# Kernel tuning notes

Hardware: AMD Instinct MI355X
Metric: run time of the kernel (lower is better)

## Reference

```python
import jax, jax.numpy as jnp
import numpy as np

L, C, H = 12, 1024, 16  # n_layer, n_embd, n_head
D = C // H
EPS = 1e-5

def gelu_new(x):
    # GPT-2 tanh-approximate GELU
    return 0.5 * x * (1.0 + jnp.tanh(np.sqrt(2.0 / np.pi).astype(np.float32) * (x + 0.044715 * x ** 3)))

def layernorm(x, g, b):
    mu = jnp.mean(x, axis=-1, keepdims=True)
    var = jnp.mean(jnp.square(x - mu), axis=-1, keepdims=True)
    return (x - mu) * jax.lax.rsqrt(var + EPS) * g + b

def setup_inputs() -> dict:
    key = jax.random.key(0)
    ks = jax.random.split(key, 8)
    std = 0.02
    inp = {
        'inputs_embeds': jax.random.normal(ks[0], (1, 1024, C), jnp.float32),
        'attention_mask': jnp.ones((1, 1024), jnp.float32),
        'ln1_g': jnp.ones((L, C), jnp.float32), 'ln1_b': jnp.zeros((L, C), jnp.float32),
        'Wqkv': jax.random.normal(ks[1], (L, C, 3 * C), jnp.float32) * std,
        'bqkv': jnp.zeros((L, 3 * C), jnp.float32),
        'Wo': jax.random.normal(ks[2], (L, C, C), jnp.float32) * (std / np.sqrt(2 * L)),
        'bo': jnp.zeros((L, C), jnp.float32),
        'ln2_g': jnp.ones((L, C), jnp.float32), 'ln2_b': jnp.zeros((L, C), jnp.float32),
        'Wfc': jax.random.normal(ks[3], (L, C, 4 * C), jnp.float32) * std,
        'bfc': jnp.zeros((L, 4 * C), jnp.float32),
        'Wmp': jax.random.normal(ks[4], (L, 4 * C, C), jnp.float32) * (std / np.sqrt(2 * L)),
        'bmp': jnp.zeros((L, C), jnp.float32),
        'lnf_g': jnp.ones((C,), jnp.float32), 'lnf_b': jnp.zeros((C,), jnp.float32),
    }
    return inp

def reference(inputs_embeds, attention_mask, ln1_g, ln1_b, Wqkv, bqkv, Wo, bo,
              ln2_g, ln2_b, Wfc, bfc, Wmp, bmp, lnf_g, lnf_b):
    B, T, _ = inputs_embeds.shape
    # padding mask -> additive bias [B,1,1,T] (broadcasts over heads and query dim)
    mask_add = -1e9 * (1.0 - attention_mask)[:, None, None, :]
    scale = 1.0 / np.sqrt(D).astype(np.float32)

    def block(x, p):
        g1, b1, Wq, bq, Wo_, bo_, g2, b2, Wf, bf, Wm, bm = p
        h = layernorm(x, g1, b1)
        qkv = h @ Wq + bq                                  # [B,T,3C]
        q, k, v = jnp.split(qkv, 3, axis=-1)
        q = q.reshape(B, T, H, D).transpose(0, 2, 1, 3)    # [B,H,T,D]
        k = k.reshape(B, T, H, D).transpose(0, 2, 1, 3)
        v = v.reshape(B, T, H, D).transpose(0, 2, 1, 3)
        att = jnp.einsum('bhqd,bhkd->bhqk', q, k) * scale + mask_add
        att = jax.nn.softmax(att, axis=-1)
        y = jnp.einsum('bhqk,bhkd->bhqd', att, v)
        y = y.transpose(0, 2, 1, 3).reshape(B, T, C)
        x = x + (y @ Wo_ + bo_)
        h2 = layernorm(x, g2, b2)
        x = x + (gelu_new(h2 @ Wf + bf) @ Wm + bm)
        return x, None

    params = (ln1_g, ln1_b, Wqkv, bqkv, Wo, bo, ln2_g, ln2_b, Wfc, bfc, Wmp, bmp)
    x, _ = jax.lax.scan(block, inputs_embeds, params)
    return layernorm(x, lnf_g, lnf_b)
```

## Files before the change

kernel.cpp:

```cpp
#include <hip/hip_runtime.h>
#include <hip/hip_bf16.h>
#include <math.h>

#define LN_EPS 1e-5f

typedef unsigned short u16;
typedef __attribute__((ext_vector_type(8))) _Float16 f16x8;
typedef __attribute__((ext_vector_type(4))) float f32x4;

__device__ __forceinline__ u16 f2h(float x) {
    _Float16 h = (_Float16)x;
    return __builtin_bit_cast(u16, h);
}
__device__ __forceinline__ void stv(float* p, float v) { *p = v; }
__device__ __forceinline__ void stv(u16* p, float v) { *p = f2h(v); }

__device__ __forceinline__ float gelu_f(float x) {
    const float kA = 0.7978845608028654f;
    return 0.5f * x * (1.f + tanhf(kA * (x + 0.044715f * x * x * x)));
}

__device__ __forceinline__ void gl_lds16(const u16* g, u16* l) {
    __builtin_amdgcn_global_load_lds(
        (const __attribute__((address_space(1))) unsigned int*)g,
        (__attribute__((address_space(3))) unsigned int*)l, 16, 0, 0);
}
template <int N> __device__ __forceinline__ void s_vmcnt() {
    asm volatile("s_waitcnt vmcnt(%0)" :: "n"(N) : "memory");
}
__device__ __forceinline__ void s_lgkm0() {
    asm volatile("s_waitcnt lgkmcnt(0)" ::: "memory");
    __builtin_amdgcn_sched_barrier(0);
}
__device__ __forceinline__ void bar() { __builtin_amdgcn_s_barrier(); }
__device__ __forceinline__ void sfence() { __builtin_amdgcn_sched_barrier(0); }

template <typename OT>
__global__ __launch_bounds__(256) void ln_kernel(const float* __restrict__ x,
                                                 const float* __restrict__ gam,
                                                 const float* __restrict__ bet,
                                                 OT* __restrict__ out) {
    int row = blockIdx.x;
    const float* xr = x + (size_t)row * 1024;
    float v[4];
    float s = 0.f, ss = 0.f;
#pragma unroll
    for (int i = 0; i < 4; i++) {
        float t = xr[threadIdx.x + i * 256];
        v[i] = t; s += t; ss += t * t;
    }
    __shared__ float r1[256], r2[256];
    r1[threadIdx.x] = s; r2[threadIdx.x] = ss;
    __syncthreads();
    for (int off = 128; off > 0; off >>= 1) {
        if (threadIdx.x < off) {
            r1[threadIdx.x] += r1[threadIdx.x + off];
            r2[threadIdx.x] += r2[threadIdx.x + off];
        }
        __syncthreads();
    }
    float mu = r1[0] * (1.f / 1024.f);
    float var = r2[0] * (1.f / 1024.f) - mu * mu;
    float rstd = rsqrtf(var + LN_EPS);
#pragma unroll
    for (int i = 0; i < 4; i++) {
        int c = threadIdx.x + i * 256;
        stv(&out[(size_t)row * 1024 + c], (v[i] - mu) * rstd * gam[c] + bet[c]);
    }
}

__global__ __launch_bounds__(256) void tr_cvt_all(
    const float* __restrict__ Wqkv, const float* __restrict__ Wo,
    const float* __restrict__ Wfc, const float* __restrict__ Wmp,
    u16* __restrict__ wqT, u16* __restrict__ woT,
    u16* __restrict__ wfT, u16* __restrict__ wmT) {
    int id = blockIdx.x;
    const float* W; u16* Wt; int K, N, idx;
    if (id < 768)       { W = Wqkv; Wt = wqT; K = 1024; N = 3072; idx = id; }
    else if (id < 1024) { W = Wo;   Wt = woT; K = 1024; N = 1024; idx = id - 768; }
    else if (id < 2048) { W = Wfc;  Wt = wfT; K = 1024; N = 4096; idx = id - 1024; }
    else                { W = Wmp;  Wt = wmT; K = 4096; N = 1024; idx = id - 2048; }
    int ntn = N >> 6;
    int n0 = (idx % ntn) * 64, k0 = (idx / ntn) * 64;

    __shared__ float tile[64][65];
    int t = threadIdx.x;
    int r = t >> 4, c4 = (t & 15) * 4;
#pragma unroll
    for (int p = 0; p < 4; p++) {
        float4 v = *(const float4*)(W + (size_t)(k0 + p * 16 + r) * N + n0 + c4);
        tile[p * 16 + r][c4 + 0] = v.x;
        tile[p * 16 + r][c4 + 1] = v.y;
        tile[p * 16 + r][c4 + 2] = v.z;
        tile[p * 16 + r][c4 + 3] = v.w;
    }
    __syncthreads();
#pragma unroll
    for (int p = 0; p < 4; p++) {
        int n = p * 16 + r;
        ushort4 o;
        o.x = f2h(tile[c4 + 0][n]);
        o.y = f2h(tile[c4 + 1][n]);
        o.z = f2h(tile[c4 + 2][n]);
        o.w = f2h(tile[c4 + 3][n]);
        *(ushort4*)(Wt + (size_t)(n0 + n) * K + k0 + c4) = o;
    }
}

template <int BM, int BN, int BK, int ACT, int RES, int WVT, typename OT>
__global__ __launch_bounds__(256) void gemm_f16(
    const u16* __restrict__ A, const u16* __restrict__ Bt,
    const float* __restrict__ bias, const float* __restrict__ res,
    OT* __restrict__ out, u16* __restrict__ vTout, int M, int N, int K) {
    __shared__ u16 As[2][BM * BK];
    __shared__ u16 Bs[2][BN * BK];
    constexpr int WM = BM / 2, WN = BN / 2;
    constexpr int FM = WM / 16, FN = WN / 16;
    constexpr int NKF = BK / 32;
    constexpr int SLOTS = BK / 8;
    constexpr int ACH = BM * BK / 8 / 256;
    constexpr int BCH = BN * BK / 8 / 256;
    constexpr int LPS = ACH + BCH;
    int tid = threadIdx.x;
    int w = tid >> 6, l = tid & 63;
    int wm = w >> 1, wn = w & 1;
    int lr = l & 15, g = l >> 4;
    int m0 = blockIdx.y * BM, n0 = blockIdx.x * BN;

    f32x4 acc[FM][FN] = {};

    auto stage = [&](int buf, int k0) {
#pragma unroll
        for (int i = 0; i < ACH; i++) {
            int chunk = i * 256 + tid;
            int row = chunk / SLOTS, s = chunk % SLOTS, sg = s ^ (row & 7);
            gl_lds16(A + (size_t)(m0 + row) * K + k0 + sg * 8, &As[buf][chunk * 8]);
        }
#pragma unroll
        for (int i = 0; i < BCH; i++) {
            int chunk = i * 256 + tid;
            int row = chunk / SLOTS, s = chunk % SLOTS, sg = s ^ (row & 7);
            gl_lds16(Bt + (size_t)(n0 + row) * K + k0 + sg * 8, &Bs[buf][chunk * 8]);
        }
    };

    int NT = K / BK;
    stage(0, 0);
    int cur = 0;
    for (int t = 0; t < NT; t++) {
        if (t + 1 < NT) { stage(cur ^ 1, (t + 1) * BK); s_vmcnt<LPS>(); }
        else            { s_vmcnt<0>(); }
        bar();
        sfence();

        const u16* Ab = &As[cur][0];
        const u16* Bb = &Bs[cur][0];
        f16x8 af[FM][NKF], bfrag[FN][NKF];
#pragma unroll
        for (int m = 0; m < FM; m++)
#pragma unroll
            for (int kf = 0; kf < NKF; kf++) {
                int row = wm * WM + m * 16 + lr;
                af[m][kf] = *(const f16x8*)(Ab + row * BK + (((kf * 4 + g) ^ (row & 7)) * 8));
            }
#pragma unroll
        for (int n = 0; n < FN; n++)
#pragma unroll
            for (int kf = 0; kf < NKF; kf++) {
                int row = wn * WN + n * 16 + lr;
                bfrag[n][kf] = *(const f16x8*)(Bb + row * BK + (((kf * 4 + g) ^ (row & 7)) * 8));
            }
#pragma unroll
        for (int kf = 0; kf < NKF; kf++)
#pragma unroll
            for (int m = 0; m < FM; m++)
#pragma unroll
                for (int n = 0; n < FN; n++)
                    acc[m][n] = __builtin_amdgcn_mfma_f32_16x16x32_f16(
                        af[m][kf], bfrag[n][kf], acc[m][n], 0, 0, 0);

        sfence();
        bar();
        cur ^= 1;
    }

#pragma unroll
    for (int m = 0; m < FM; m++) {
#pragma unroll
        for (int n = 0; n < FN; n++) {
            int col = n0 + wn * WN + n * 16 + lr;
            int row0 = m0 + wm * WM + m * 16 + 4 * g;
            float bv = bias[col];
            u16 hv[4];
#pragma unroll
            for (int r = 0; r < 4; r++) {
                float v = acc[m][n][r] + bv;
                if (ACT) v = gelu_f(v);
                if (RES) v += res[(size_t)(row0 + r) * N + col];
                stv(&out[(size_t)(row0 + r) * N + col], v);
                hv[r] = f2h(v);
            }
            if (WVT && col >= 2048) {
                ushort4 pv; pv.x = hv[0]; pv.y = hv[1]; pv.z = hv[2]; pv.w = hv[3];
                *(ushort4*)(vTout + (size_t)(col - 2048) * 1024 + row0) = pv;
            }
        }
    }
}

__global__ __launch_bounds__(256) void attn_mfma(
    const u16* __restrict__ qkv, const u16* __restrict__ vT,
    const float* __restrict__ mask, u16* __restrict__ y) {
    int h = blockIdx.y;
    int q0 = blockIdx.x * 64;
    int tid = threadIdx.x;
    int w = tid >> 6, l = tid & 63;
    int lr = l & 15, g = l >> 4;

    __shared__ u16 Ks[2][128 * 64];
    __shared__ u16 Vs[2][64 * 128];
    __shared__ u16 Ps[4 * 16 * 128];
    __shared__ float maskb[1024];

    for (int i = tid; i < 1024; i += 256) maskb[i] = -1e9f * (1.f - mask[i]);
    s_lgkm0();

    f16x8 qf[2];
#pragma unroll
    for (int kf = 0; kf < 2; kf++)
        qf[kf] = *(const f16x8*)(qkv + (size_t)(q0 + w * 16 + lr) * 3072 + h * 64 + kf * 32 + g * 8);

    f32x4 o[4] = {};
    float mrow[4], lrow[4];
#pragma unroll
    for (int r = 0; r < 4; r++) { mrow[r] = -1e30f; lrow[r] = 0.f; }

    u16* Psw = Ps + w * 2048;

    auto stage = [&](int buf, int kc) {
#pragma unroll
        for (int i = 0; i < 4; i++) {
            int chunk = i * 256 + tid;
            int krow = chunk >> 3, ks = chunk & 7, ksg = ks ^ (krow & 7);
            gl_lds16(qkv + (size_t)(kc * 128 + krow) * 3072 + 1024 + h * 64 + ksg * 8,
                     &Ks[buf][chunk * 8]);
            int vrow = chunk >> 4, vs = chunk & 15, vsg = vs ^ (vrow & 7);
            gl_lds16(vT + (size_t)(h * 64 + vrow) * 1024 + kc * 128 + vsg * 8,
                     &Vs[buf][chunk * 8]);
        }
    };

    stage(0, 0);
    int cur = 0;
    for (int kc = 0; kc < 8; kc++) {
        if (kc + 1 < 8) { stage(cur ^ 1, kc + 1); s_vmcnt<8>(); }
        else            { s_vmcnt<0>(); }
        bar();
        sfence();
        const u16* Kb = &Ks[cur][0];
        const u16* Vb = &Vs[cur][0];

        f32x4 s[8] = {};
        __builtin_amdgcn_s_setprio(1);
#pragma unroll
        for (int n = 0; n < 8; n++)
#pragma unroll
            for (int kf = 0; kf < 2; kf++) {
                int row = n * 16 + lr;
                f16x8 kfrag = *(const f16x8*)(Kb + row * 64 + (((kf * 4 + g) ^ (row & 7)) * 8));
                s[n] = __builtin_amdgcn_mfma_f32_16x16x32_f16(qf[kf], kfrag, s[n], 0, 0, 0);
            }
        __builtin_amdgcn_s_setprio(0);

        float mcol[8];
#pragma unroll
        for (int n = 0; n < 8; n++) mcol[n] = maskb[kc * 128 + n * 16 + lr];

        float scl[4], mnew[4], psum[4];
#pragma unroll
        for (int r = 0; r < 4; r++) {
            float mx = -1e30f;
#pragma unroll
            for (int n = 0; n < 8; n++) {
                float sv = s[n][r] * 0.125f + mcol[n];
                s[n][r] = sv;
                mx = fmaxf(mx, sv);
            }
            mx = fmaxf(mx, __shfl_xor(mx, 1));
            mx = fmaxf(mx, __shfl_xor(mx, 2));
            mx = fmaxf(mx, __shfl_xor(mx, 4));
            mx = fmaxf(mx, __shfl_xor(mx, 8));
            mnew[r] = fmaxf(mrow[r], mx);
            scl[r] = __expf(mrow[r] - mnew[r]);
            mrow[r] = mnew[r];
            psum[r] = 0.f;
        }
#pragma unroll
        for (int n = 0; n < 8; n++) {
            float p0 = __expf(s[n][0] - mnew[0]);
            float p1 = __expf(s[n][1] - mnew[1]);
            float p2 = __expf(s[n][2] - mnew[2]);
            float p3 = __expf(s[n][3] - mnew[3]);
            psum[0] += p0; psum[1] += p1; psum[2] += p2; psum[3] += p3;
            int col = n * 16 + lr, cs = col >> 3, cl = col & 7;
            int r0 = 4 * g;
            Psw[(r0 + 0) * 128 + ((cs ^ ((r0 + 0) & 7)) * 8) + cl] = f2h(p0);
            Psw[(r0 + 1) * 128 + ((cs ^ ((r0 + 1) & 7)) * 8) + cl] = f2h(p1);
            Psw[(r0 + 2) * 128 + ((cs ^ ((r0 + 2) & 7)) * 8) + cl] = f2h(p2);
            Psw[(r0 + 3) * 128 + ((cs ^ ((r0 + 3) & 7)) * 8) + cl] = f2h(p3);
        }
#pragma unroll
        for (int r = 0; r < 4; r++) {
            float ps_ = psum[r];
            ps_ += __shfl_xor(ps_, 1);
            ps_ += __shfl_xor(ps_, 2);
            ps_ += __shfl_xor(ps_, 4);
            ps_ += __shfl_xor(ps_, 8);
            lrow[r] = lrow[r] * scl[r] + ps_;
#pragma unroll
            for (int dn = 0; dn < 4; dn++) o[dn][r] *= scl[r];
        }

        f16x8 pa[4];
#pragma unroll
        for (int kf = 0; kf < 4; kf++)
            pa[kf] = *(const f16x8*)(Psw + lr * 128 + (((kf * 4 + g) ^ (lr & 7)) * 8));
        __builtin_amdgcn_s_setprio(1);
#pragma unroll
        for (int dn = 0; dn < 4; dn++) {
#pragma unroll
            for (int kf = 0; kf < 4; kf++) {
                int row = dn * 16 + lr;
                f16x8 vb = *(const f16x8*)(Vb + row * 128 + (((kf * 4 + g) ^ (row & 7)) * 8));
                o[dn] = __builtin_amdgcn_mfma_f32_16x16x32_f16(pa[kf], vb, o[dn], 0, 0, 0);
            }
        }
        __builtin_amdgcn_s_setprio(0);

        sfence();
        bar();
        cur ^= 1;
    }

    float inv[4];
#pragma unroll
    for (int r = 0; r < 4; r++) inv[r] = 1.f / lrow[r];
#pragma unroll
    for (int dn = 0; dn < 4; dn++)
#pragma unroll
        for (int r = 0; r < 4; r++) {
            int row = q0 + w * 16 + 4 * g + r;
            int col = h * 64 + dn * 16 + lr;
            y[(size_t)row * 1024 + col] = f2h(o[dn][r] * inv[r]);
        }
}

extern "C" void kernel_launch(void* const* d_in, const int* in_sizes, int n_in,
                              void* d_out, int out_size, void* d_ws, size_t ws_size,
                              hipStream_t stream) {
    const float* inputs_embeds = (const float*)d_in[0];
    const float* attn_mask     = (const float*)d_in[1];
    const float* ln1_g = (const float*)d_in[2];
    const float* ln1_b = (const float*)d_in[3];
    const float* Wqkv  = (const float*)d_in[4];
    const float* bqkv  = (const float*)d_in[5];
    const float* Wo    = (const float*)d_in[6];
    const float* bo    = (const float*)d_in[7];
    const float* ln2_g = (const float*)d_in[8];
    const float* ln2_b = (const float*)d_in[9];
    const float* Wfc   = (const float*)d_in[10];
    const float* bfc   = (const float*)d_in[11];
    const float* Wmp   = (const float*)d_in[12];
    const float* bmp   = (const float*)d_in[13];
    const float* lnf_g = (const float*)d_in[14];
    const float* lnf_b = (const float*)d_in[15];
    float* out = (float*)d_out;

    char* ws = (char*)d_ws;
    float* x   = (float*)ws;
    u16* hbuf  = (u16*)(ws + (4u << 20));
    u16* qkvb  = (u16*)(ws + (6u << 20));
    u16* fcb   = qkvb;
    u16* ybuf  = hbuf;
    u16* wqT   = (u16*)(ws + (14u << 20));
    u16* woT   = (u16*)(ws + (20u << 20));
    u16* wfT   = (u16*)(ws + (22u << 20));
    u16* wmT   = (u16*)(ws + (30u << 20));
    u16* vTb   = (u16*)(ws + (38u << 20));

    hipMemcpyAsync(x, inputs_embeds, (size_t)(1 << 20) * sizeof(float),
                   hipMemcpyDeviceToDevice, stream);

    for (int l = 0; l < 12; l++) {
        tr_cvt_all<<<3072, 256, 0, stream>>>(
            Wqkv + (size_t)l * 1024 * 3072, Wo + (size_t)l * 1024 * 1024,
            Wfc + (size_t)l * 1024 * 4096, Wmp + (size_t)l * 4096 * 1024,
            wqT, woT, wfT, wmT);

        ln_kernel<u16><<<1024, 256, 0, stream>>>(x, ln1_g + l * 1024, ln1_b + l * 1024, hbuf);
        gemm_f16<64, 128, 64, 0, 0, 1, u16><<<dim3(24, 16), 256, 0, stream>>>(
            hbuf, wqT, bqkv + (size_t)l * 3072, nullptr, qkvb, vTb, 1024, 3072, 1024);
        attn_mfma<<<dim3(16, 16), 256, 0, stream>>>(qkvb, vTb, attn_mask, ybuf);
        gemm_f16<64, 64, 128, 0, 1, 0, float><<<dim3(16, 16), 256, 0, stream>>>(
            ybuf, woT, bo + (size_t)l * 1024, x, x, nullptr, 1024, 1024, 1024);
        ln_kernel<u16><<<1024, 256, 0, stream>>>(x, ln2_g + l * 1024, ln2_b + l * 1024, hbuf);
        gemm_f16<128, 128, 64, 1, 0, 0, u16><<<dim3(32, 8), 256, 0, stream>>>(
            hbuf, wfT, bfc + (size_t)l * 4096, nullptr, fcb, nullptr, 1024, 4096, 1024);
        gemm_f16<64, 64, 128, 0, 1, 0, float><<<dim3(16, 16), 256, 0, stream>>>(
            fcb, wmT, bmp + (size_t)l * 1024, x, x, nullptr, 1024, 1024, 4096);
    }
    ln_kernel<float><<<1024, 256, 0, stream>>>(x, lnf_g, lnf_b, out);
}
```

Measured before the change: 1.598 ms.

## Split-K with atomic accumulation for output and MLP-proj GEMMs

Adds a SPLITK template parameter and a RES==2 epilogue that atomically adds partial sums into the fp32 residual stream, with bias added only by the first K-slice. The Wo and Wmp projections switch to 128x128 tiles split along K across 4 and 8 slices, so the residual add comes for free from accumulating into x. Launch bounds now request 2 blocks per CU. The goal is more parallel blocks and larger tiles for the narrow N=1024 GEMMs, at the cost of atomic traffic and nondeterministic summation order.

```diff
diff --git a/kernel.cpp b/kernel.cpp
--- a/kernel.cpp
+++ b/kernel.cpp
@@ -107,8 +107,8 @@
     }
 }
 
-template <int BM, int BN, int BK, int ACT, int RES, int WVT, typename OT>
-__global__ __launch_bounds__(256) void gemm_f16(
+template <int BM, int BN, int BK, int ACT, int RES, int WVT, int SPLITK, typename OT>
+__global__ __launch_bounds__(256, 2) void gemm_f16(
     const u16* __restrict__ A, const u16* __restrict__ Bt,
     const float* __restrict__ bias, const float* __restrict__ res,
     OT* __restrict__ out, u16* __restrict__ vTout, int M, int N, int K) {
@@ -126,6 +126,8 @@
     int wm = w >> 1, wn = w & 1;
     int lr = l & 15, g = l >> 4;
     int m0 = blockIdx.y * BM, n0 = blockIdx.x * BN;
+    int kbase = (SPLITK > 1) ? blockIdx.z * (K / SPLITK) : 0;
+    int Kc = (SPLITK > 1) ? (K / SPLITK) : K;
 
     f32x4 acc[FM][FN] = {};
 
@@ -134,17 +136,17 @@
         for (int i = 0; i < ACH; i++) {
             int chunk = i * 256 + tid;
             int row = chunk / SLOTS, s = chunk % SLOTS, sg = s ^ (row & 7);
-            gl_lds16(A + (size_t)(m0 + row) * K + k0 + sg * 8, &As[buf][chunk * 8]);
+            gl_lds16(A + (size_t)(m0 + row) * K + kbase + k0 + sg * 8, &As[buf][chunk * 8]);
         }
 #pragma unroll
         for (int i = 0; i < BCH; i++) {
             int chunk = i * 256 + tid;
             int row = chunk / SLOTS, s = chunk % SLOTS, sg = s ^ (row & 7);
-            gl_lds16(Bt + (size_t)(n0 + row) * K + k0 + sg * 8, &Bs[buf][chunk * 8]);
+            gl_lds16(Bt + (size_t)(n0 + row) * K + kbase + k0 + sg * 8, &Bs[buf][chunk * 8]);
         }
     };
 
-    int NT = K / BK;
+    int NT = Kc / BK;
     stage(0, 0);
     int cur = 0;
     for (int t = 0; t < NT; t++) {
@@ -194,11 +196,16 @@
             u16 hv[4];
 #pragma unroll
             for (int r = 0; r < 4; r++) {
-                float v = acc[m][n][r] + bv;
-                if (ACT) v = gelu_f(v);
-                if (RES) v += res[(size_t)(row0 + r) * N + col];
-                stv(&out[(size_t)(row0 + r) * N + col], v);
-                hv[r] = f2h(v);
+                if (RES == 2) {
+                    float v = acc[m][n][r] + ((SPLITK > 1 && blockIdx.z != 0) ? 0.f : bv);
+                    atomicAdd((float*)&out[(size_t)(row0 + r) * N + col], v);
+                } else {
+                    float v = acc[m][n][r] + bv;
+                    if (ACT) v = gelu_f(v);
+                    if (RES == 1) v += res[(size_t)(row0 + r) * N + col];
+                    stv(&out[(size_t)(row0 + r) * N + col], v);
+                    hv[r] = f2h(v);
+                }
             }
             if (WVT && col >= 2048) {
                 ushort4 pv; pv.x = hv[0]; pv.y = hv[1]; pv.z = hv[2]; pv.w = hv[3];
@@ -398,16 +405,16 @@
             wqT, woT, wfT, wmT);
 
         ln_kernel<u16><<<1024, 256, 0, stream>>>(x, ln1_g + l * 1024, ln1_b + l * 1024, hbuf);
-        gemm_f16<64, 128, 64, 0, 0, 1, u16><<<dim3(24, 16), 256, 0, stream>>>(
+        gemm_f16<64, 128, 64, 0, 0, 1, 1, u16><<<dim3(24, 16), 256, 0, stream>>>(
             hbuf, wqT, bqkv + (size_t)l * 3072, nullptr, qkvb, vTb, 1024, 3072, 1024);
         attn_mfma<<<dim3(16, 16), 256, 0, stream>>>(qkvb, vTb, attn_mask, ybuf);
-        gemm_f16<64, 64, 128, 0, 1, 0, float><<<dim3(16, 16), 256, 0, stream>>>(
-            ybuf, woT, bo + (size_t)l * 1024, x, x, nullptr, 1024, 1024, 1024);
+        gemm_f16<128, 128, 64, 0, 2, 0, 4, float><<<dim3(8, 8, 4), 256, 0, stream>>>(
+            ybuf, woT, bo + (size_t)l * 1024, nullptr, x, nullptr, 1024, 1024, 1024);
         ln_kernel<u16><<<1024, 256, 0, stream>>>(x, ln2_g + l * 1024, ln2_b + l * 1024, hbuf);
-        gemm_f16<128, 128, 64, 1, 0, 0, u16><<<dim3(32, 8), 256, 0, stream>>>(
+        gemm_f16<128, 128, 64, 1, 0, 0, 1, u16><<<dim3(32, 8), 256, 0, stream>>>(
             hbuf, wfT, bfc + (size_t)l * 4096, nullptr, fcb, nullptr, 1024, 4096, 1024);
-        gemm_f16<64, 64, 128, 0, 1, 0, float><<<dim3(16, 16), 256, 0, stream>>>(
-            fcb, wmT, bmp + (size_t)l * 1024, x, x, nullptr, 1024, 1024, 4096);
+        gemm_f16<128, 128, 64, 0, 2, 0, 8, float><<<dim3(8, 8, 8), 256, 0, stream>>>(
+            fcb, wmT, bmp + (size_t)l * 1024, nullptr, x, nullptr, 1024, 1024, 4096);
     }
     ln_kernel<float><<<1024, 256, 0, stream>>>(x, lnf_g, lnf_b, out);
 }
```

After: 1.748 ms. 9.4% more time.

## Fuse layernorm into GEMM A-loads and batch weight conversion across layers

Applied to the files above, without the earlier changes.

Drops the separate layernorm kernels. The QKV and FC GEMMs now compute per-row mean and rstd from fp32 x in a prologue, then normalize and convert A tiles to fp16 while staging them into LDS. The per-layer weight transpose and convert is also replaced by one launch covering all 12 layers when the workspace is large enough, leaving fewer small launches. The cost is redundant row statistics and fp32 A reads in every N-tile block, and A staging becomes synchronous register loads instead of async global-to-LDS copies.

```diff
diff --git a/kernel.cpp b/kernel.cpp
--- a/kernel.cpp
+++ b/kernel.cpp
@@ -72,14 +72,18 @@
 __global__ __launch_bounds__(256) void tr_cvt_all(
     const float* __restrict__ Wqkv, const float* __restrict__ Wo,
     const float* __restrict__ Wfc, const float* __restrict__ Wmp,
-    u16* __restrict__ wqT, u16* __restrict__ woT,
-    u16* __restrict__ wfT, u16* __restrict__ wmT) {
+    u16* __restrict__ wq, u16* __restrict__ wo,
+    u16* __restrict__ wf, u16* __restrict__ wm) {
+    size_t lf = (size_t)blockIdx.y;
+    Wqkv += lf * 3145728; Wo += lf * 1048576; Wfc += lf * 4194304; Wmp += lf * 4194304;
+    wq += lf * 12582912; wo += lf * 12582912; wf += lf * 12582912; wm += lf * 12582912;
+
     int id = blockIdx.x;
     const float* W; u16* Wt; int K, N, idx;
-    if (id < 768)       { W = Wqkv; Wt = wqT; K = 1024; N = 3072; idx = id; }
-    else if (id < 1024) { W = Wo;   Wt = woT; K = 1024; N = 1024; idx = id - 768; }
-    else if (id < 2048) { W = Wfc;  Wt = wfT; K = 1024; N = 4096; idx = id - 1024; }
-    else                { W = Wmp;  Wt = wmT; K = 4096; N = 1024; idx = id - 2048; }
+    if (id < 768)       { W = Wqkv; Wt = wq; K = 1024; N = 3072; idx = id; }
+    else if (id < 1024) { W = Wo;   Wt = wo; K = 1024; N = 1024; idx = id - 768; }
+    else if (id < 2048) { W = Wfc;  Wt = wf; K = 1024; N = 4096; idx = id - 1024; }
+    else                { W = Wmp;  Wt = wm; K = 4096; N = 1024; idx = id - 2048; }
     int ntn = N >> 6;
     int n0 = (idx % ntn) * 64, k0 = (idx / ntn) * 64;
 
@@ -107,34 +111,92 @@
     }
 }
 
-template <int BM, int BN, int BK, int ACT, int RES, int WVT, typename OT>
+template <int BM, int BN, int BK, int ACT, int RES, int WVT, int LNA, typename OT>
 __global__ __launch_bounds__(256) void gemm_f16(
-    const u16* __restrict__ A, const u16* __restrict__ Bt,
+    const void* __restrict__ Av, const u16* __restrict__ Bt,
     const float* __restrict__ bias, const float* __restrict__ res,
-    OT* __restrict__ out, u16* __restrict__ vTout, int M, int N, int K) {
+    OT* __restrict__ out, u16* __restrict__ vTout,
+    const float* __restrict__ lng, const float* __restrict__ lnb,
+    int M, int N, int K) {
     __shared__ u16 As[2][BM * BK];
     __shared__ u16 Bs[2][BN * BK];
+    __shared__ float r1[256], r2[256];
+    __shared__ float rowmu[BM], rowrs[BM];
     constexpr int WM = BM / 2, WN = BN / 2;
     constexpr int FM = WM / 16, FN = WN / 16;
     constexpr int NKF = BK / 32;
     constexpr int SLOTS = BK / 8;
     constexpr int ACH = BM * BK / 8 / 256;
     constexpr int BCH = BN * BK / 8 / 256;
-    constexpr int LPS = ACH + BCH;
+    constexpr int LPS = LNA ? BCH : (ACH + BCH);
     int tid = threadIdx.x;
     int w = tid >> 6, l = tid & 63;
     int wm = w >> 1, wn = w & 1;
     int lr = l & 15, g = l >> 4;
     int m0 = blockIdx.y * BM, n0 = blockIdx.x * BN;
 
+    float amu[ACH], ars[ACH];
+    if (LNA) {
+        constexpr int TPR = 256 / BM;
+        constexpr int CPT = 1024 / TPR;
+        int row = tid / TPR, seg = tid % TPR;
+        const float* xr = ((const float*)Av) + (size_t)(m0 + row) * 1024 + seg * CPT;
+        float s = 0.f, ss = 0.f;
+        for (int c = 0; c < CPT; c += 4) {
+            float4 v4 = *(const float4*)(xr + c);
+            s += v4.x + v4.y + v4.z + v4.w;
+            ss += v4.x * v4.x + v4.y * v4.y + v4.z * v4.z + v4.w * v4.w;
+        }
+        r1[tid] = s; r2[tid] = ss;
+        __syncthreads();
+        if (seg == 0) {
+#pragma unroll
+            for (int t = 1; t < TPR; t++) { s += r1[tid + t]; ss += r2[tid + t]; }
+            float mu = s * (1.f / 1024.f);
+            float var = ss * (1.f / 1024.f) - mu * mu;
+            rowmu[row] = mu; rowrs[row] = rsqrtf(var + LN_EPS);
+        }
+        __syncthreads();
+#pragma unroll
+        for (int i = 0; i < ACH; i++) {
+            int arow = (i * 256 + tid) / SLOTS;
+            amu[i] = rowmu[arow]; ars[i] = rowrs[arow];
+        }
+    }
+
     f32x4 acc[FM][FN] = {};
 
     auto stage = [&](int buf, int k0) {
-#pragma unroll
-        for (int i = 0; i < ACH; i++) {
-            int chunk = i * 256 + tid;
-            int row = chunk / SLOTS, s = chunk % SLOTS, sg = s ^ (row & 7);
-            gl_lds16(A + (size_t)(m0 + row) * K + k0 + sg * 8, &As[buf][chunk * 8]);
+        if (LNA) {
+#pragma unroll
+            for (int i = 0; i < ACH; i++) {
+                int chunk = i * 256 + tid;
+                int row = chunk / SLOTS, s = chunk % SLOTS;
+                int c0 = k0 + s * 8;
+                const float* xp = ((const float*)Av) + (size_t)(m0 + row) * 1024 + c0;
+                float4 a0 = *(const float4*)xp, a1 = *(const float4*)(xp + 4);
+                float4 g0 = *(const float4*)(lng + c0), g1 = *(const float4*)(lng + c0 + 4);
+                float4 b0 = *(const float4*)(lnb + c0), b1 = *(const float4*)(lnb + c0 + 4);
+                float mu = amu[i], rs = ars[i];
+                f16x8 hv;
+                hv[0] = (_Float16)((a0.x - mu) * rs * g0.x + b0.x);
+                hv[1] = (_Float16)((a0.y - mu) * rs * g0.y + b0.y);
+                hv[2] = (_Float16)((a0.z - mu) * rs * g0.z + b0.z);
+                hv[3] = (_Float16)((a0.w - mu) * rs * g0.w + b0.w);
+                hv[4] = (_Float16)((a1.x - mu) * rs * g1.x + b1.x);
+                hv[5] = (_Float16)((a1.y - mu) * rs * g1.y + b1.y);
+                hv[6] = (_Float16)((a1.z - mu) * rs * g1.z + b1.z);
+                hv[7] = (_Float16)((a1.w - mu) * rs * g1.w + b1.w);
+                *(f16x8*)(&As[buf][row * BK + ((s ^ (row & 7)) * 8)]) = hv;
+            }
+        } else {
+            const u16* A = (const u16*)Av;
+#pragma unroll
+            for (int i = 0; i < ACH; i++) {
+                int chunk = i * 256 + tid;
+                int row = chunk / SLOTS, s = chunk % SLOTS, sg = s ^ (row & 7);
+                gl_lds16(A + (size_t)(m0 + row) * K + k0 + sg * 8, &As[buf][chunk * 8]);
+            }
         }
 #pragma unroll
         for (int i = 0; i < BCH; i++) {
@@ -146,6 +208,7 @@
 
     int NT = K / BK;
     stage(0, 0);
+    if (LNA) s_lgkm0();
     int cur = 0;
     for (int t = 0; t < NT; t++) {
         if (t + 1 < NT) { stage(cur ^ 1, (t + 1) * BK); s_vmcnt<LPS>(); }
@@ -378,36 +441,50 @@
 
     char* ws = (char*)d_ws;
     float* x   = (float*)ws;
-    u16* hbuf  = (u16*)(ws + (4u << 20));
+    u16* ybuf  = (u16*)(ws + (4u << 20));
     u16* qkvb  = (u16*)(ws + (6u << 20));
     u16* fcb   = qkvb;
-    u16* ybuf  = hbuf;
-    u16* wqT   = (u16*)(ws + (14u << 20));
-    u16* woT   = (u16*)(ws + (20u << 20));
-    u16* wfT   = (u16*)(ws + (22u << 20));
-    u16* wmT   = (u16*)(ws + (30u << 20));
-    u16* vTb   = (u16*)(ws + (38u << 20));
+    u16* vTb   = (u16*)(ws + (14u << 20));
+    u16* wbase = (u16*)(ws + (16u << 20));
+
+    const size_t WPL = 12582912;
+    bool big = ws_size >= (16ull << 20) + 12ull * WPL * 2;
 
     hipMemcpyAsync(x, inputs_embeds, (size_t)(1 << 20) * sizeof(float),
                    hipMemcpyDeviceToDevice, stream);
 
+    if (big) {
+        tr_cvt_all<<<dim3(3072, 12), 256, 0, stream>>>(
+            Wqkv, Wo, Wfc, Wmp,
+            wbase, wbase + 3145728, wbase + 4194304, wbase + 8388608);
+    }
+
     for (int l = 0; l < 12; l++) {
-        tr_cvt_all<<<3072, 256, 0, stream>>>(
-            Wqkv + (size_t)l * 1024 * 3072, Wo + (size_t)l * 1024 * 1024,
-            Wfc + (size_t)l * 1024 * 4096, Wmp + (size_t)l * 4096 * 1024,
-            wqT, woT, wfT, wmT);
-
-        ln_kernel<u16><<<1024, 256, 0, stream>>>(x, ln1_g + l * 1024, ln1_b + l * 1024, hbuf);
-        gemm_f16<64, 128, 64, 0, 0, 1, u16><<<dim3(24, 16), 256, 0, stream>>>(
-            hbuf, wqT, bqkv + (size_t)l * 3072, nullptr, qkvb, vTb, 1024, 3072, 1024);
+        u16 *wq, *wo_, *wf, *wm;
+        if (big) {
+            u16* wl = wbase + (size_t)l * WPL;
+            wq = wl; wo_ = wl + 3145728; wf = wl + 4194304; wm = wl + 8388608;
+        } else {
+            wq = wbase; wo_ = wbase + 3145728; wf = wbase + 4194304; wm = wbase + 8388608;
+            tr_cvt_all<<<dim3(3072, 1), 256, 0, stream>>>(
+                Wqkv + (size_t)l * 3145728, Wo + (size_t)l * 1048576,
+                Wfc + (size_t)l * 4194304, Wmp + (size_t)l * 4194304,
+                wq, wo_, wf, wm);
+        }
+
+        gemm_f16<64, 128, 64, 0, 0, 1, 1, u16><<<dim3(24, 16), 256, 0, stream>>>(
+            x, wq, bqkv + (size_t)l * 3072, nullptr, qkvb, vTb,
+            ln1_g + l * 1024, ln1_b + l * 1024, 1024, 3072, 1024);
         attn_mfma<<<dim3(16, 16), 256, 0, stream>>>(qkvb, vTb, attn_mask, ybuf);
-        gemm_f16<64, 64, 128, 0, 1, 0, float><<<dim3(16, 16), 256, 0, stream>>>(
-            ybuf, woT, bo + (size_t)l * 1024, x, x, nullptr, 1024, 1024, 1024);
-        ln_kernel<u16><<<1024, 256, 0, stream>>>(x, ln2_g + l * 1024, ln2_b + l * 1024, hbuf);
-        gemm_f16<128, 128, 64, 1, 0, 0, u16><<<dim3(32, 8), 256, 0, stream>>>(
-            hbuf, wfT, bfc + (size_t)l * 4096, nullptr, fcb, nullptr, 1024, 4096, 1024);
-        gemm_f16<64, 64, 128, 0, 1, 0, float><<<dim3(16, 16), 256, 0, stream>>>(
-            fcb, wmT, bmp + (size_t)l * 1024, x, x, nullptr, 1024, 1024, 4096);
+        gemm_f16<64, 64, 128, 0, 1, 0, 0, float><<<dim3(16, 16), 256, 0, stream>>>(
+            ybuf, wo_, bo + (size_t)l * 1024, x, x, nullptr, nullptr, nullptr,
+            1024, 1024, 1024);
+        gemm_f16<128, 128, 64, 1, 0, 0, 1, u16><<<dim3(32, 8), 256, 0, stream>>>(
+            x, wf, bfc + (size_t)l * 4096, nullptr, fcb, nullptr,
+            ln2_g + l * 1024, ln2_b + l * 1024, 1024, 4096, 1024);
+        gemm_f16<64, 64, 128, 0, 1, 0, 0, float><<<dim3(16, 16), 256, 0, stream>>>(
+            fcb, wm, bmp + (size_t)l * 1024, x, x, nullptr, nullptr, nullptr,
+            1024, 1024, 4096);
     }
     ln_kernel<float><<<1024, 256, 0, stream>>>(x, lnf_g, lnf_b, out);
 }
```

After: 2.159 ms. 1.35x slower.
